# Kernel optimization log

Hardware: AMD Instinct MI355X
Metric: run time of the kernel (lower is better)

## Reference

```python
import jax, jax.numpy as jnp
import numpy as np
from jax import lax

V_PATCH = (1, 2, 3, 4, 5, 6, 8, 10, 13, 16)
BETA = 0.25
RESI = 0.5          # abs(quant_resi): h*(1-r) + conv(h)*r
K_PHI = 4           # share_quant_resi
PHI_TICKS = np.linspace(1.0 / (3 * K_PHI), 1.0 - 1.0 / (3 * K_PHI), K_PHI)


def _area_mat(out_s, in_s):
    # torch F.interpolate(mode='area') == adaptive avg pool: row-stochastic matrix
    M = np.zeros((out_s, in_s), np.float32)
    for i in range(out_s):
        s = (i * in_s) // out_s
        e = -((-(i + 1) * in_s) // out_s)  # ceil((i+1)*in/out)
        M[i, s:e] = 1.0 / (e - s)
    return jnp.asarray(M)


def _bicubic_mat(out_s, in_s):
    # torch bicubic, align_corners=False, a=-0.75, border-clamped taps
    a = -0.75
    i = np.arange(out_s)
    src = (i + 0.5) * in_s / out_s - 0.5
    fl = np.floor(src)
    M = np.zeros((out_s, in_s), np.float32)
    for t in range(-1, 3):
        x = np.abs(src - (fl + t))
        w = np.where(x <= 1.0, (a + 2) * x**3 - (a + 3) * x**2 + 1.0,
                     np.where(x < 2.0, a * x**3 - 5 * a * x**2 + 8 * a * x - 4 * a, 0.0))
        idx = np.clip(fl + t, 0, in_s - 1).astype(int)
        np.add.at(M, (i, idx), w)
    return jnp.asarray(M)


def _resize(x, M):
    # separable resize on square maps: x [B,C,h,w] -> [B,C,o,o]
    x = jnp.einsum('oh,bchw->bcow', M, x)
    return jnp.einsum('pw,bcow->bcop', M, x)


def _phi(h, w, b):
    # Phi: Conv2d(C,C,3,pad=1); out = h*(1-r) + conv(h)*r
    c = lax.conv_general_dilated(h, w, (1, 1), 'SAME',
                                 dimension_numbers=('NCHW', 'OIHW', 'NCHW'))
    c = c + b[None, :, None, None]
    return h * (1.0 - RESI) + c * RESI


def setup_inputs() -> dict:
    key = jax.random.key(0)
    k1, k2, k3, k4 = jax.random.split(key, 4)
    f = jax.random.normal(k1, (128, 32, 16, 16), jnp.float32)
    emb = jax.random.normal(k2, (4096, 32), jnp.float32) * 0.1
    phi_w = jax.random.normal(k3, (4, 32, 32, 3, 3), jnp.float32) * 0.05
    phi_b = jax.random.normal(k4, (4, 32), jnp.float32) * 0.01
    return {"f_BChw": f, "emb_W": emb, "phi_W": phi_w, "phi_b": phi_b}


def reference(f_BChw, emb_W, phi_W, phi_b):
    B, C, H, W = f_BChw.shape
    SN = len(V_PATCH)
    f = f_BChw.astype(jnp.float32)
    f_ng = lax.stop_gradient(f)
    f_rest = f_ng
    f_hat = jnp.zeros_like(f_ng)
    emb_ng = lax.stop_gradient(emb_W)         # torch uses embedding.weight.data
    e_sq = jnp.sum(emb_ng**2, axis=1)          # [V]
    loss = jnp.float32(0.0)
    idx_list = []
    for si, pn in enumerate(V_PATCH):
        rest = f_rest if si == SN - 1 else _resize(f_rest, _area_mat(pn, H))
        rest_NC = rest.transpose(0, 2, 3, 1).reshape(-1, C)      # [B*pn*pn, C]
        d = jnp.sum(rest_NC**2, axis=1, keepdims=True) + e_sq - 2.0 * (rest_NC @ emb_ng.T)
        idx = jnp.argmin(d, axis=1)                              # [B*pn*pn]
        idx_list.append(idx)
        h = emb_W[idx].reshape(B, pn, pn, C).transpose(0, 3, 1, 2)  # differentiable gather
        if si != SN - 1:
            h = _resize(h, _bicubic_mat(H, pn))
        k = int(np.argmin(np.abs(PHI_TICKS - si / (SN - 1))))
        h = _phi(h, phi_W[k], phi_b[k])
        f_hat = f_hat + h
        f_rest = f_rest - h
        loss = loss + BETA * jnp.mean((lax.stop_gradient(f_hat) - f)**2) \
                    + jnp.mean((f_hat - f_ng)**2)
    loss = loss / SN
    f_hat_out = lax.stop_gradient(f_hat) - f_ng + f  # straight-through
    return (f_hat_out, loss, jnp.concatenate(idx_list))
```

## Files before the change

kernel.cpp:

```cpp
#include <hip/hip_runtime.h>
#include <hip/hip_bf16.h>
#include <math.h>


#define B_  128
#define V_  4096
#define SN_ 10
#define NPIX_ (B_*32*256)

#define WS_FREST   0
#define WS_SLOTA   1048576
#define WS_SLOTB   1114112
#define WS_ESQ     1179648
#define WS_TW      1183744
#define WS_TI      1184320
#define WS_LOSSP   1184896
#define WS_RESTH   1187456
#define WS_RESTM   1711744
#define WS_RESTL   2236032
#define WS_EMBH    2760320
#define WS_EMBM    2825856
#define WS_EMBL    2891392
#define WS_WSPL    2956928

typedef __attribute__((ext_vector_type(8))) short short8_t;
typedef __attribute__((ext_vector_type(4))) float f32x4;
typedef unsigned long long ull;
#define MFMA(a,b,c) __builtin_amdgcn_mfma_f32_16x16x32_bf16((a),(b),(c),0,0,0)

__device__ inline void gl_lds16(const void* g, void* l) {
  __builtin_amdgcn_global_load_lds((const __attribute__((address_space(1))) void*)g,
                                   (__attribute__((address_space(3))) void*)l, 16, 0, 0);
}
__device__ inline void gl_lds4(const void* g, void* l) {
  __builtin_amdgcn_global_load_lds((const __attribute__((address_space(1))) void*)g,
                                   (__attribute__((address_space(3))) void*)l, 4, 0, 0);
}

__device__ inline void split3(float a, ushort* h, ushort* m, ushort* l) {
  unsigned ua = __float_as_uint(a);
  ushort uh = (ushort)(ua >> 16);
  float fh = __uint_as_float((unsigned)uh << 16);
  float r1 = a - fh;
  ushort um = (ushort)(__float_as_uint(r1) >> 16);
  float fm = __uint_as_float((unsigned)um << 16);
  float r2 = r1 - fm;
  ushort ul = (ushort)(__float_as_uint(r2) >> 16);
  *h = uh; *m = um; *l = ul;
}

__device__ inline short8_t s8_from_laneM1(short8_t v) {
  union { short8_t s; unsigned u[4]; } a, r;
  a.s = v;
#pragma unroll
  for (int i = 0; i < 4; ++i)
    r.u[i] = __builtin_amdgcn_update_dpp(0u, a.u[i], 0x111, 0xF, 0xF, true);
  return r.s;
}
__device__ inline short8_t s8_from_laneP1(short8_t v) {
  union { short8_t s; unsigned u[4]; } a, r;
  a.s = v;
#pragma unroll
  for (int i = 0; i < 4; ++i)
    r.u[i] = __builtin_amdgcn_update_dpp(0u, a.u[i], 0x101, 0xF, 0xF, true);
  return r.s;
}


__global__ __launch_bounds__(256) void k_prep(const float* __restrict__ emb,
                                              float* __restrict__ esq,
                                              ushort* __restrict__ eh,
                                              ushort* __restrict__ em,
                                              ushort* __restrict__ el,
                                              float* __restrict__ tw,
                                              int* __restrict__ ti,
                                              ull* __restrict__ slotA) {
  int bx = blockIdx.x, t = threadIdx.x;
  if (bx < 16) {
    int v = bx * 256 + t;
    const float4* e4 = (const float4*)(emb + (size_t)v * 32);
    float s = 0.f;
#pragma unroll
    for (int half = 0; half < 4; ++half) {
      float4 x0 = e4[half * 2], x1 = e4[half * 2 + 1];
      s += x0.x * x0.x + x0.y * x0.y + x0.z * x0.z + x0.w * x0.w;
      s += x1.x * x1.x + x1.y * x1.y + x1.z * x1.z + x1.w * x1.w;
      float xs[8] = {x0.x, x0.y, x0.z, x0.w, x1.x, x1.y, x1.z, x1.w};
      ushort hs[8], ms[8], ls[8];
#pragma unroll
      for (int j = 0; j < 8; ++j) split3(xs[j], &hs[j], &ms[j], &ls[j]);
      uint4 ph, pm, pl;
      ph.x = (unsigned)hs[0] | ((unsigned)hs[1] << 16); ph.y = (unsigned)hs[2] | ((unsigned)hs[3] << 16);
      ph.z = (unsigned)hs[4] | ((unsigned)hs[5] << 16); ph.w = (unsigned)hs[6] | ((unsigned)hs[7] << 16);
      pm.x = (unsigned)ms[0] | ((unsigned)ms[1] << 16); pm.y = (unsigned)ms[2] | ((unsigned)ms[3] << 16);
      pm.z = (unsigned)ms[4] | ((unsigned)ms[5] << 16); pm.w = (unsigned)ms[6] | ((unsigned)ms[7] << 16);
      pl.x = (unsigned)ls[0] | ((unsigned)ls[1] << 16); pl.y = (unsigned)ls[2] | ((unsigned)ls[3] << 16);
      pl.z = (unsigned)ls[4] | ((unsigned)ls[5] << 16); pl.w = (unsigned)ls[6] | ((unsigned)ls[7] << 16);
      ((uint4*)(eh + (size_t)v * 32))[half] = ph;
      ((uint4*)(em + (size_t)v * 32))[half] = pm;
      ((uint4*)(el + (size_t)v * 32))[half] = pl;
    }
    esq[v] = -0.5f * s;
  } else {
    if (t < 128) slotA[t] = 0ULL;
    if (t >= 144) return;
    const int pns[9] = {1, 2, 3, 4, 5, 6, 8, 10, 13};
    int si = t / 16, Y = t % 16;
    int pn = pns[si];
    double src = (Y + 0.5) * (double)pn / 16.0 - 0.5;
    double fl = floor(src);
    const double a = -0.75;
#pragma unroll
    for (int k = 0; k < 4; ++k) {
      double x = fabs(src - (fl + (k - 1)));
      double w;
      if (x <= 1.0)      w = (a + 2.0) * x * x * x - (a + 3.0) * x * x + 1.0;
      else if (x < 2.0)  w = a * x * x * x - 5.0 * a * x * x + 8.0 * a * x - 4.0 * a;
      else               w = 0.0;
      int id = (int)fl + (k - 1);
      id = id < 0 ? 0 : (id > pn - 1 ? pn - 1 : id);
      tw[si * 64 + Y * 4 + k] = (float)w;
      ti[si * 64 + Y * 4 + k] = id;
    }
  }
}

__global__ __launch_bounds__(256) void k_prep2(const float* __restrict__ f,
                                               const float* __restrict__ phiW,
                                               ushort* __restrict__ rh,
                                               ushort* __restrict__ rm,
                                               ushort* __restrict__ rl,
                                               ushort* __restrict__ wspl) {
  int bx = blockIdx.x, t = threadIdx.x;
  if (bx < 16) {
    int i = bx * 256 + t;
    int phi = i >> 10, o = (i >> 5) & 31, ci = i & 31;
    const float* src = phiW + (((size_t)phi * 32 + o) * 32 + ci) * 9;
    ushort* dst = wspl + (size_t)phi * 27648;
#pragma unroll
    for (int q = 0; q < 9; ++q) {
      ushort uh, um, ul;
      split3(src[q], &uh, &um, &ul);
      dst[(size_t)(0 * 9 + q) * 1024 + o * 32 + ci] = uh;
      dst[(size_t)(9 + q) * 1024 + o * 32 + ci] = um;
      dst[(size_t)(18 + q) * 1024 + o * 32 + ci] = ul;
    }
  } else {
    int tid = (bx - 16) * 256 + t;
    int c = tid & 31, n = tid >> 5;
    const float* base = f + ((size_t)n * 32 + c) * 256;
    float s = 0.f;
    for (int yy = 0; yy < 16; ++yy)
      for (int xx = 0; xx < 16; ++xx) s += base[yy * 16 + xx];
    float a = s * ((1.0f / 16.0f) * (1.0f / 16.0f));
    ushort uh, um, ul;
    split3(a, &uh, &um, &ul);
    rh[(size_t)n * 32 + c] = uh;
    rm[(size_t)n * 32 + c] = um;
    rl[(size_t)n * 32 + c] = ul;
  }
}

template<int R>
__global__ __launch_bounds__(256) void k_nn(const ushort* __restrict__ rest_h,
                                            const ushort* __restrict__ rest_m,
                                            const ushort* __restrict__ rest_l,
                                            const ushort* __restrict__ emb_h,
                                            const ushort* __restrict__ emb_m,
                                            const ushort* __restrict__ emb_l,
                                            const float* __restrict__ esq_g,
                                            ull* __restrict__ slot,
                                            int rows, int S, int cps) {
  __shared__ ushort lb[2][3][2048];
  __shared__ float les[2][64];
  const int t = threadIdx.x;
  const int w = t >> 6;
  const int col = t & 15;
  const int g = (t >> 4) & 3;
  const int sp = blockIdx.y;
  const int rowbase = blockIdx.x * (64 * R);

  auto stage = [&](int bf, int ch) {
    int cb = sp * cps + ch * 64;
    int code = cb + (t >> 2);
    int u = (t & 3) ^ ((code ^ (code >> 2)) & 3);
    size_t off = (size_t)code * 32 + (size_t)u * 8;
    gl_lds16(emb_h + off, &lb[bf][0][w * 512]);
    gl_lds16(emb_m + off, &lb[bf][1][w * 512]);
    gl_lds16(emb_l + off, &lb[bf][2][w * 512]);
    if ((t & 63) < 16) gl_lds4(esq_g + cb + w * 16 + (t & 15), &les[bf][w * 16]);
  };

  stage(0, 0);

  short8_t ah[R], am[R], al[R];
#pragma unroll
  for (int rt = 0; rt < R; ++rt) {
    int n = rowbase + (w * R + rt) * 16 + col;
    if (n >= rows) n = rows - 1;
    size_t o = (size_t)n * 32 + g * 8;
    ah[rt] = *(const short8_t*)(rest_h + o);
    am[rt] = *(const short8_t*)(rest_m + o);
    al[rt] = *(const short8_t*)(rest_l + o);
  }

  float best[R][4];
  int bidx[R][4];
#pragma unroll
  for (int rt = 0; rt < R; ++rt)
#pragma unroll
    for (int r = 0; r < 4; ++r) { best[rt][r] = -3.4e38f; bidx[rt][r] = 0x7fffffff; }

  const int NC = cps >> 6;
  int buf = 0;
  for (int ch = 0; ch < NC; ++ch) {
    if (ch + 1 < NC) {
      stage(buf ^ 1, ch + 1);
      asm volatile("s_waitcnt vmcnt(4)" ::: "memory");
    } else {
      asm volatile("s_waitcnt vmcnt(0)" ::: "memory");
    }
    __builtin_amdgcn_s_barrier();

    int cb0 = sp * cps + ch * 64;
#pragma unroll
    for (int s4 = 0; s4 < 4; ++s4) {
      int cl = s4 * 16 + col;
      int slotbase = (cl * 4 + (g ^ ((cl ^ (cl >> 2)) & 3))) * 8;
      short8_t bh  = *(const short8_t*)&lb[buf][0][slotbase];
      short8_t bm  = *(const short8_t*)&lb[buf][1][slotbase];
      short8_t bl2 = *(const short8_t*)&lb[buf][2][slotbase];
      float es = les[buf][cl];
      f32x4 c0 = {es, es, es, es};
      f32x4 acc[R];
#pragma unroll
      for (int rt = 0; rt < R; ++rt) acc[rt] = MFMA(ah[rt], bh, c0);
#pragma unroll
      for (int rt = 0; rt < R; ++rt) acc[rt] = MFMA(ah[rt], bm, acc[rt]);
#pragma unroll
      for (int rt = 0; rt < R; ++rt) acc[rt] = MFMA(am[rt], bh, acc[rt]);
#pragma unroll
      for (int rt = 0; rt < R; ++rt) acc[rt] = MFMA(ah[rt], bl2, acc[rt]);
#pragma unroll
      for (int rt = 0; rt < R; ++rt) acc[rt] = MFMA(am[rt], bm, acc[rt]);
#pragma unroll
      for (int rt = 0; rt < R; ++rt) acc[rt] = MFMA(al[rt], bh, acc[rt]);
      int code = cb0 + cl;
#pragma unroll
      for (int rt = 0; rt < R; ++rt)
#pragma unroll
        for (int r = 0; r < 4; ++r)
          if (acc[rt][r] > best[rt][r]) { best[rt][r] = acc[rt][r]; bidx[rt][r] = code; }
    }
    __syncthreads();
    buf ^= 1;
  }

#pragma unroll
  for (int rt = 0; rt < R; ++rt)
#pragma unroll
    for (int r = 0; r < 4; ++r) {
      float bd = best[rt][r];
      int bi = bidx[rt][r];
#pragma unroll
      for (int mm2 = 1; mm2 < 16; mm2 <<= 1) {
        float od = __shfl_xor(bd, mm2, 16);
        int oi = __shfl_xor(bi, mm2, 16);
        if (od > bd || (od == bd && oi < bi)) { bd = od; bi = oi; }
      }
      if ((t & 15) == 0) {
        int rown = rowbase + (w * R + rt) * 16 + g * 4 + r;
        if (rown < rows) {
          unsigned mu = __float_as_uint(bd);
          mu ^= (mu & 0x80000000u) ? 0xFFFFFFFFu : 0x80000000u;
          ull key = ((ull)mu << 32) | (unsigned)(~bi);
          atomicMax(&slot[rown], key);
        }
      }
    }
}

template<bool LAST>
__global__ __launch_bounds__(1024) void k_scale(const ull* __restrict__ slot_in,
                                                ull* __restrict__ slot_next,
                                                const float* __restrict__ emb,
                                                const float* __restrict__ tw,
                                                const int* __restrict__ ti,
                                                const ushort* __restrict__ wspl,
                                                const float* __restrict__ bias,
                                                const float* __restrict__ f,
                                                const float* __restrict__ fr_in,
                                                float* __restrict__ fr_out,
                                                float* __restrict__ fhat_out,
                                                float* __restrict__ out_idx_f,
                                                float* __restrict__ lossp,
                                                ushort* __restrict__ rh,
                                                ushort* __restrict__ rm,
                                                ushort* __restrict__ rl,
                                                int pn, int si, int pn_next,
                                                int rows_next) {
  __shared__ ushort h_bf[3][256][40];
  __shared__ float hsm[32 * 177];
  __shared__ float xt[32][208];
  __shared__ float h_my[16][260];
  __shared__ ushort w_lds[27][16][36];
  __shared__ int ci_s[256];
  __shared__ float redw[16];
  float* poolb = hsm;

  const int b = blockIdx.x;
  const int cog = blockIdx.y * 16;
  const int t = threadIdx.x;
  const int pn2 = pn * pn;
  const int w = t >> 6, l = t & 63;
  const int X = l & 15, kq = l >> 4;
  const int pix = w * 16 + X;

  float fr_old[4], f_old[4];
#pragma unroll
  for (int r = 0; r < 4; ++r) {
    size_t ga = ((size_t)b * 32 + cog + kq * 4 + r) * 256 + pix;
    fr_old[r] = fr_in[ga];
    f_old[r] = LAST ? f[ga] : 0.f;
  }
  for (int i = t; i < 1728; i += 1024) {
    int seg = i & 3;
    int o = (i >> 2) & 15;
    int lq = i >> 6;
    const ushort* src = wspl + ((size_t)lq * 32 + cog + o) * 32 + seg * 8;
    *(short8_t*)&w_lds[lq][o][seg * 8] = *(const short8_t*)src;
  }
  for (int rem = t; rem < pn2; rem += 1024) {
    ull sv = slot_in[b * pn2 + rem];
    int code = (int)(~(unsigned)sv);
    ci_s[rem] = code;
    out_idx_f[b * pn2 + rem] = (float)code;
  }
  __syncthreads();

#pragma unroll
  for (int cc = 0; cc < 2; ++cc) {
    int c = 2 * w + cc;
    if (LAST) {
      for (int p2 = l; p2 < 256; p2 += 64) {
        float v = emb[(size_t)ci_s[p2] * 32 + c];
        ushort uh, um, ul; split3(v, &uh, &um, &ul);
        h_bf[0][p2][c] = uh; h_bf[1][p2][c] = um; h_bf[2][p2][c] = ul;
        int cl = c - cog;
        if ((unsigned)cl < 16u) h_my[cl][p2] = v;
      }
    } else {
      for (int rem = l; rem < pn2; rem += 64)
        hsm[c * 177 + rem] = emb[(size_t)ci_s[rem] * 32 + c];
      asm volatile("s_waitcnt lgkmcnt(0)" ::: "memory");
      for (int i = l; i < pn * 16; i += 64) {
        int Xi = i & 15, y = i >> 4;
        float a = 0.f;
#pragma unroll
        for (int u = 0; u < 4; ++u)
          a += tw[si * 64 + Xi * 4 + u] * hsm[c * 177 + y * pn + ti[si * 64 + Xi * 4 + u]];
        xt[c][y * 16 + Xi] = a;
      }
      asm volatile("s_waitcnt lgkmcnt(0)" ::: "memory");
      for (int p2 = l; p2 < 256; p2 += 64) {
        int Xi = p2 & 15, Y = p2 >> 4;
        float a = 0.f;
#pragma unroll
        for (int u = 0; u < 4; ++u)
          a += tw[si * 64 + Y * 4 + u] * xt[c][ti[si * 64 + Y * 4 + u] * 16 + Xi];
        ushort uh, um, ul; split3(a, &uh, &um, &ul);
        h_bf[0][p2][c] = uh; h_bf[1][p2][c] = um; h_bf[2][p2][c] = ul;
        int cl = c - cog;
        if ((unsigned)cl < 16u) h_my[cl][p2] = a;
      }
    }
  }
  __syncthreads();

  f32x4 accA, accB;
#pragma unroll
  for (int r = 0; r < 4; ++r) {
    accA[r] = bias[cog + kq * 4 + r];
    accB[r] = 0.f;
  }

  for (int dy = 0; dy < 3; ++dy) {
    int Yp = w + dy - 1;
    bool ok = (Yp >= 0 && Yp < 16);
    short8_t bc[3];
    if (ok) {
#pragma unroll
      for (int lv = 0; lv < 3; ++lv)
        bc[lv] = *(const short8_t*)&h_bf[lv][Yp * 16 + X][kq * 8];
    }
#pragma unroll
    for (int dx = 0; dx < 3; ++dx) {
      int q = dy * 3 + dx;
      short8_t aH = *(const short8_t*)&w_lds[0 * 9 + q][l & 15][kq * 8];
      short8_t aM = *(const short8_t*)&w_lds[9 + q][l & 15][kq * 8];
      short8_t aL = *(const short8_t*)&w_lds[18 + q][l & 15][kq * 8];
      if (!ok) continue;
      short8_t bH = bc[0], bM = bc[1], bL = bc[2];
      if (dx == 0) { bH = s8_from_laneM1(bH); bM = s8_from_laneM1(bM); bL = s8_from_laneM1(bL); }
      else if (dx == 2) { bH = s8_from_laneP1(bH); bM = s8_from_laneP1(bM); bL = s8_from_laneP1(bL); }
      accA = MFMA(aH, bH, accA);
      accB = MFMA(aH, bM, accB);
      accA = MFMA(aM, bH, accA);
      accB = MFMA(aH, bL, accB);
      accA = MFMA(aM, bM, accA);
      accB = MFMA(aL, bH, accB);
    }
  }

  float lsum = 0.f;
#pragma unroll
  for (int r = 0; r < 4; ++r) {
    int ol = kq * 4 + r;
    float convv = accA[r] + accB[r];
    float outv = 0.5f * h_my[ol][pix] + 0.5f * convv;
    float nf = fr_old[r] - outv;
    size_t ga = ((size_t)b * 32 + cog + ol) * 256 + pix;
    if (LAST) {
      fhat_out[ga] = f_old[r] - nf;
    } else {
      fr_out[ga] = nf;
      poolb[ol * 256 + pix] = nf;
    }
    lsum += nf * nf;
  }

  if (!LAST) {
    __syncthreads();
    int pn2n = pn_next * pn_next;
    for (int i = t; i < 16 * pn2n; i += 1024) {
      int o = i / pn2n, rem = i - o * pn2n;
      int y = rem / pn_next, x = rem - y * pn_next;
      int sy = (y * 16) / pn_next, ey = ((y + 1) * 16 + pn_next - 1) / pn_next;
      int sx = (x * 16) / pn_next, ex = ((x + 1) * 16 + pn_next - 1) / pn_next;
      float s = 0.f;
      for (int yy = sy; yy < ey; ++yy)
        for (int xx = sx; xx < ex; ++xx) s += poolb[o * 256 + yy * 16 + xx];
      float a = s * ((1.0f / (float)(ey - sy)) * (1.0f / (float)(ex - sx)));
      ushort uh, um, ul;
      split3(a, &uh, &um, &ul);
      size_t n = (size_t)b * pn2n + rem;
      rh[n * 32 + cog + o] = uh;
      rm[n * 32 + cog + o] = um;
      rl[n * 32 + cog + o] = ul;
    }
    int blk = b * 2 + blockIdx.y;
    int stride = (rows_next + 255) >> 8;
    int base = blk * stride;
    for (int i = t; i < stride; i += 1024) {
      int s = base + i;
      if (s < rows_next) slot_next[s] = 0ULL;
    }
  }

#pragma unroll
  for (int off = 32; off > 0; off >>= 1) lsum += __shfl_down(lsum, off);
  if (l == 0) redw[w] = lsum;
  __syncthreads();
  if (t == 0) {
    float s2 = 0.f;
#pragma unroll
    for (int i = 0; i < 16; ++i) s2 += redw[i];
    lossp[si * 256 + blockIdx.y * 128 + b] = s2;
  }
}

__global__ __launch_bounds__(256) void k_lossfin(const float* __restrict__ part,
                                                 float* __restrict__ out) {
  int t = threadIdx.x;
  float s = 0.f;
  for (int i = t; i < SN_ * 256; i += 256) s += part[i];
  __shared__ float red[256];
  red[t] = s;
  __syncthreads();
  for (int o = 128; o > 0; o >>= 1) {
    if (t < o) red[t] += red[t + o];
    __syncthreads();
  }
  if (t == 0) out[NPIX_] = red[0] * (1.25f / (10.0f * (float)NPIX_));
}


static void compute_phi_k(int* ks) {
  const int K = 4;
  double start = 1.0 / (3.0 * K);
  double stop = 1.0 - 1.0 / (3.0 * K);
  double step = (stop - start) / (K - 1);
  double ticks[4];
  for (int i = 0; i < K; ++i) ticks[i] = (double)i * step + start;
  ticks[K - 1] = stop;
  for (int si = 0; si < SN_; ++si) {
    double x = (double)si / (SN_ - 1);
    int best = 0;
    double bd = fabs(ticks[0] - x);
    for (int i = 1; i < K; ++i) {
      double d = fabs(ticks[i] - x);
      if (d < bd) { bd = d; best = i; }
    }
    ks[si] = best;
  }
}

extern "C" void kernel_launch(void* const* d_in, const int* in_sizes, int n_in,
                              void* d_out, int out_size, void* d_ws, size_t ws_size,
                              hipStream_t stream) {
  (void)in_sizes; (void)n_in; (void)out_size; (void)ws_size;
  const float* f    = (const float*)d_in[0];
  const float* emb  = (const float*)d_in[1];
  const float* phiW = (const float*)d_in[2];
  const float* phiB = (const float*)d_in[3];
  float* out = (float*)d_out;
  float* ws = (float*)d_ws;

  float* f_rest = ws + WS_FREST;
  ull*   slotA  = (ull*)(ws + WS_SLOTA);
  ull*   slotB  = (ull*)(ws + WS_SLOTB);
  float* esq    = ws + WS_ESQ;
  float* tw     = ws + WS_TW;
  int*   ti     = (int*)(ws + WS_TI);
  float* lossp  = ws + WS_LOSSP;
  ushort* rest_h = (ushort*)(ws + WS_RESTH);
  ushort* rest_m = (ushort*)(ws + WS_RESTM);
  ushort* rest_l = (ushort*)(ws + WS_RESTL);
  ushort* emb_h  = (ushort*)(ws + WS_EMBH);
  ushort* emb_m  = (ushort*)(ws + WS_EMBM);
  ushort* emb_l  = (ushort*)(ws + WS_EMBL);
  ushort* wspl   = (ushort*)(ws + WS_WSPL);

  static const int pns[SN_] = {1, 2, 3, 4, 5, 6, 8, 10, 13, 16};
  static const int Rs[SN_]  = {1, 1, 1, 2, 2, 2, 4, 4, 4, 4};
  static const int Ss[SN_]  = {64, 64, 32, 32, 16, 16, 16, 16, 8, 4};
  int ks[SN_];
  compute_phi_k(ks);

  k_prep<<<17, 256, 0, stream>>>(emb, esq, emb_h, emb_m, emb_l, tw, ti, slotA);
  k_prep2<<<32, 256, 0, stream>>>(f, phiW, rest_h, rest_m, rest_l, wspl);

  int idx_off = 0;
  for (int si = 0; si < SN_; ++si) {
    int pn = pns[si];
    int pn2 = pn * pn;
    int rows = B_ * pn2;
    int R = Rs[si], S = Ss[si];
    int cps = V_ / S;
    int rowblocks = (rows + 64 * R - 1) / (64 * R);
    ull* slot_cur  = (si & 1) ? slotB : slotA;
    ull* slot_nxt  = (si & 1) ? slotA : slotB;

    dim3 grid(rowblocks, S);
    if (R == 1)
      k_nn<1><<<grid, 256, 0, stream>>>(rest_h, rest_m, rest_l, emb_h, emb_m, emb_l,
                                        esq, slot_cur, rows, S, cps);
    else if (R == 2)
      k_nn<2><<<grid, 256, 0, stream>>>(rest_h, rest_m, rest_l, emb_h, emb_m, emb_l,
                                        esq, slot_cur, rows, S, cps);
    else
      k_nn<4><<<grid, 256, 0, stream>>>(rest_h, rest_m, rest_l, emb_h, emb_m, emb_l,
                                        esq, slot_cur, rows, S, cps);

    bool last = (si == SN_ - 1);
    int pn_next = last ? 0 : pns[si + 1];
    int rows_next = last ? 0 : B_ * pn_next * pn_next;
    const ushort* wsp = wspl + (size_t)ks[si] * 27648;
    const float* bi = phiB + (size_t)ks[si] * 32;
    if (last)
      k_scale<true><<<dim3(B_, 2), 1024, 0, stream>>>(
          slot_cur, slot_nxt, emb, tw, ti, wsp, bi, f,
          f_rest, f_rest, out,
          out + NPIX_ + 1 + idx_off, lossp,
          rest_h, rest_m, rest_l, pn, si, pn_next, rows_next);
    else
      k_scale<false><<<dim3(B_, 2), 1024, 0, stream>>>(
          slot_cur, slot_nxt, emb, tw, ti, wsp, bi, f,
          (si == 0) ? f : f_rest, f_rest, nullptr,
          out + NPIX_ + 1 + idx_off, lossp,
          rest_h, rest_m, rest_l, pn, si, pn_next, rows_next);
    idx_off += rows;
  }

  k_lossfin<<<1, 256, 0, stream>>>(lossp, out);
}
```

Baseline: 390.1 us.

## Split per-scale kernel into separate interpolation and conv kernels via global scratch

The fused per-scale kernel is split into two kernels. k_interp gathers codebook rows, does the bicubic upsample and writes the bf16 triple-split and fp32 maps to workspace. k_conv then reads those maps and the conv weights straight from global memory instead of staging them in LDS. This removes the interpolation work that was duplicated across both channel-group blocks and frees LDS, at the cost of an extra launch per scale and an extra global round-trip for the intermediate maps. The pooling loop index order is also changed.

New measurement: 421.9 us. +8.1%, slower.

```diff
diff --git a/kernel.cpp b/kernel.cpp
--- a/kernel.cpp
+++ b/kernel.cpp
@@ -9,19 +9,21 @@
 #define NPIX_ (B_*32*256)
 
 #define WS_FREST   0
-#define WS_SLOTA   1048576
-#define WS_SLOTB   1114112
-#define WS_ESQ     1179648
-#define WS_TW      1183744
-#define WS_TI      1184320
-#define WS_LOSSP   1184896
-#define WS_RESTH   1187456
-#define WS_RESTM   1711744
-#define WS_RESTL   2236032
-#define WS_EMBH    2760320
-#define WS_EMBM    2825856
-#define WS_EMBL    2891392
-#define WS_WSPL    2956928
+#define WS_HF32    1048576
+#define WS_HBF     2097152
+#define WS_SLOTA   3670016
+#define WS_SLOTB   3735552
+#define WS_ESQ     3801088
+#define WS_TW      3805184
+#define WS_TI      3805760
+#define WS_LOSSP   3806336
+#define WS_RESTH   3808896
+#define WS_RESTM   4333184
+#define WS_RESTL   4857472
+#define WS_EMBH    5381760
+#define WS_EMBM    5447296
+#define WS_EMBL    5512832
+#define WS_WSPL    5578368
 
 typedef __attribute__((ext_vector_type(8))) short short8_t;
 typedef __attribute__((ext_vector_type(4))) float f32x4;
@@ -281,37 +283,107 @@
 }
 
 template<bool LAST>
-__global__ __launch_bounds__(1024) void k_scale(const ull* __restrict__ slot_in,
-                                                ull* __restrict__ slot_next,
+__global__ __launch_bounds__(256) void k_interp(const ull* __restrict__ slot_in,
                                                 const float* __restrict__ emb,
                                                 const float* __restrict__ tw,
                                                 const int* __restrict__ ti,
-                                                const ushort* __restrict__ wspl,
-                                                const float* __restrict__ bias,
-                                                const float* __restrict__ f,
-                                                const float* __restrict__ fr_in,
-                                                float* __restrict__ fr_out,
-                                                float* __restrict__ fhat_out,
                                                 float* __restrict__ out_idx_f,
-                                                float* __restrict__ lossp,
-                                                ushort* __restrict__ rh,
-                                                ushort* __restrict__ rm,
-                                                ushort* __restrict__ rl,
-                                                int pn, int si, int pn_next,
-                                                int rows_next) {
-  __shared__ ushort h_bf[3][256][40];
-  __shared__ float hsm[32 * 177];
-  __shared__ float xt[32][208];
-  __shared__ float h_my[16][260];
-  __shared__ ushort w_lds[27][16][36];
+                                                ushort* __restrict__ hb0,
+                                                ushort* __restrict__ hb1,
+                                                ushort* __restrict__ hb2,
+                                                float* __restrict__ h_f32,
+                                                int pn, int si) {
   __shared__ int ci_s[256];
+  __shared__ float hsm[8][176];
+  __shared__ float xt[8][208];
+  const int b = blockIdx.x;
+  const int c0 = blockIdx.y * 8;
+  const int t = threadIdx.x;
+  const int pn2 = pn * pn;
+
+  for (int rem = t; rem < pn2; rem += 256) {
+    ull sv = slot_in[b * pn2 + rem];
+    int code = (int)(~(unsigned)sv);
+    ci_s[rem] = code;
+    if (blockIdx.y == 0) out_idx_f[b * pn2 + rem] = (float)code;
+  }
+  __syncthreads();
+
+  float vals[8];
+  if (LAST) {
+    const float4* emb4 = (const float4*)emb;
+    int ci = ci_s[t];
+    float4 e0 = emb4[(size_t)ci * 8 + (c0 >> 2)];
+    float4 e1 = emb4[(size_t)ci * 8 + (c0 >> 2) + 1];
+    vals[0] = e0.x; vals[1] = e0.y; vals[2] = e0.z; vals[3] = e0.w;
+    vals[4] = e1.x; vals[5] = e1.y; vals[6] = e1.z; vals[7] = e1.w;
+  } else {
+    const float4* emb4 = (const float4*)emb;
+    for (int i = t; i < pn2 * 2; i += 256) {
+      int rem = i >> 1, half = i & 1;
+      float4 e = emb4[(size_t)ci_s[rem] * 8 + (c0 >> 2) + half];
+      hsm[half * 4 + 0][rem] = e.x;
+      hsm[half * 4 + 1][rem] = e.y;
+      hsm[half * 4 + 2][rem] = e.z;
+      hsm[half * 4 + 3][rem] = e.w;
+    }
+    __syncthreads();
+    int e1n = 8 * pn * 16;
+    for (int i = t; i < e1n; i += 256) {
+      int Xi = i & 15, r2 = i >> 4;
+      int y = r2 % pn, lc = r2 / pn;
+      float a = 0.f;
+#pragma unroll
+      for (int u = 0; u < 4; ++u)
+        a += tw[si * 64 + Xi * 4 + u] * hsm[lc][y * pn + ti[si * 64 + Xi * 4 + u]];
+      xt[lc][y * 16 + Xi] = a;
+    }
+    __syncthreads();
+    int Xi = t & 15, Y = t >> 4;
+#pragma unroll
+    for (int lc = 0; lc < 8; ++lc) {
+      float a = 0.f;
+#pragma unroll
+      for (int u = 0; u < 4; ++u)
+        a += tw[si * 64 + Y * 4 + u] * xt[lc][ti[si * 64 + Y * 4 + u] * 16 + Xi];
+      vals[lc] = a;
+    }
+  }
+
+  ushort hs[8], ms[8], ls[8];
+#pragma unroll
+  for (int j = 0; j < 8; ++j) split3(vals[j], &hs[j], &ms[j], &ls[j]);
+  size_t base = ((size_t)b * 256 + t) * 32 + c0;
+  *(short8_t*)(hb0 + base) = *(short8_t*)hs;
+  *(short8_t*)(hb1 + base) = *(short8_t*)ms;
+  *(short8_t*)(hb2 + base) = *(short8_t*)ls;
+  float4* hf4 = (float4*)(h_f32 + base);
+  hf4[0] = make_float4(vals[0], vals[1], vals[2], vals[3]);
+  hf4[1] = make_float4(vals[4], vals[5], vals[6], vals[7]);
+}
+
+template<bool LAST>
+__global__ __launch_bounds__(1024) void k_conv(const ushort* __restrict__ hb0,
+                                               const ushort* __restrict__ hb1,
+                                               const ushort* __restrict__ hb2,
+                                               const float* __restrict__ h_f32,
+                                               const ushort* __restrict__ wspl_k,
+                                               const float* __restrict__ bias,
+                                               const float* __restrict__ f,
+                                               const float* __restrict__ fr_in,
+                                               float* __restrict__ fr_out,
+                                               float* __restrict__ fhat_out,
+                                               float* __restrict__ lossp,
+                                               ushort* __restrict__ rh,
+                                               ushort* __restrict__ rm,
+                                               ushort* __restrict__ rl,
+                                               ull* __restrict__ slot_next,
+                                               int si, int pn_next, int rows_next) {
+  __shared__ float poolb[16 * 256];
   __shared__ float redw[16];
-  float* poolb = hsm;
-
   const int b = blockIdx.x;
   const int cog = blockIdx.y * 16;
   const int t = threadIdx.x;
-  const int pn2 = pn * pn;
   const int w = t >> 6, l = t & 63;
   const int X = l & 15, kq = l >> 4;
   const int pix = w * 16 + X;
@@ -323,59 +395,7 @@
     fr_old[r] = fr_in[ga];
     f_old[r] = LAST ? f[ga] : 0.f;
   }
-  for (int i = t; i < 1728; i += 1024) {
-    int seg = i & 3;
-    int o = (i >> 2) & 15;
-    int lq = i >> 6;
-    const ushort* src = wspl + ((size_t)lq * 32 + cog + o) * 32 + seg * 8;
-    *(short8_t*)&w_lds[lq][o][seg * 8] = *(const short8_t*)src;
-  }
-  for (int rem = t; rem < pn2; rem += 1024) {
-    ull sv = slot_in[b * pn2 + rem];
-    int code = (int)(~(unsigned)sv);
-    ci_s[rem] = code;
-    out_idx_f[b * pn2 + rem] = (float)code;
-  }
-  __syncthreads();
-
-#pragma unroll
-  for (int cc = 0; cc < 2; ++cc) {
-    int c = 2 * w + cc;
-    if (LAST) {
-      for (int p2 = l; p2 < 256; p2 += 64) {
-        float v = emb[(size_t)ci_s[p2] * 32 + c];
-        ushort uh, um, ul; split3(v, &uh, &um, &ul);
-        h_bf[0][p2][c] = uh; h_bf[1][p2][c] = um; h_bf[2][p2][c] = ul;
-        int cl = c - cog;
-        if ((unsigned)cl < 16u) h_my[cl][p2] = v;
-      }
-    } else {
-      for (int rem = l; rem < pn2; rem += 64)
-        hsm[c * 177 + rem] = emb[(size_t)ci_s[rem] * 32 + c];
-      asm volatile("s_waitcnt lgkmcnt(0)" ::: "memory");
-      for (int i = l; i < pn * 16; i += 64) {
-        int Xi = i & 15, y = i >> 4;
-        float a = 0.f;
-#pragma unroll
-        for (int u = 0; u < 4; ++u)
-          a += tw[si * 64 + Xi * 4 + u] * hsm[c * 177 + y * pn + ti[si * 64 + Xi * 4 + u]];
-        xt[c][y * 16 + Xi] = a;
-      }
-      asm volatile("s_waitcnt lgkmcnt(0)" ::: "memory");
-      for (int p2 = l; p2 < 256; p2 += 64) {
-        int Xi = p2 & 15, Y = p2 >> 4;
-        float a = 0.f;
-#pragma unroll
-        for (int u = 0; u < 4; ++u)
-          a += tw[si * 64 + Y * 4 + u] * xt[c][ti[si * 64 + Y * 4 + u] * 16 + Xi];
-        ushort uh, um, ul; split3(a, &uh, &um, &ul);
-        h_bf[0][p2][c] = uh; h_bf[1][p2][c] = um; h_bf[2][p2][c] = ul;
-        int cl = c - cog;
-        if ((unsigned)cl < 16u) h_my[cl][p2] = a;
-      }
-    }
-  }
-  __syncthreads();
+  float4 hmy = *(const float4*)(h_f32 + ((size_t)b * 256 + pix) * 32 + cog + kq * 4);
 
   f32x4 accA, accB;
 #pragma unroll
@@ -384,21 +404,24 @@
     accB[r] = 0.f;
   }
 
+#pragma unroll 1
   for (int dy = 0; dy < 3; ++dy) {
     int Yp = w + dy - 1;
     bool ok = (Yp >= 0 && Yp < 16);
     short8_t bc[3];
     if (ok) {
-#pragma unroll
-      for (int lv = 0; lv < 3; ++lv)
-        bc[lv] = *(const short8_t*)&h_bf[lv][Yp * 16 + X][kq * 8];
+      size_t hbase = ((size_t)b * 256 + Yp * 16 + X) * 32 + kq * 8;
+      bc[0] = *(const short8_t*)(hb0 + hbase);
+      bc[1] = *(const short8_t*)(hb1 + hbase);
+      bc[2] = *(const short8_t*)(hb2 + hbase);
     }
 #pragma unroll
     for (int dx = 0; dx < 3; ++dx) {
       int q = dy * 3 + dx;
-      short8_t aH = *(const short8_t*)&w_lds[0 * 9 + q][l & 15][kq * 8];
-      short8_t aM = *(const short8_t*)&w_lds[9 + q][l & 15][kq * 8];
-      short8_t aL = *(const short8_t*)&w_lds[18 + q][l & 15][kq * 8];
+      const ushort* wp = wspl_k + (size_t)q * 1024 + (size_t)(cog + (l & 15)) * 32 + kq * 8;
+      short8_t aH = *(const short8_t*)(wp);
+      short8_t aM = *(const short8_t*)(wp + 9 * 1024);
+      short8_t aL = *(const short8_t*)(wp + 18 * 1024);
       if (!ok) continue;
       short8_t bH = bc[0], bM = bc[1], bL = bc[2];
       if (dx == 0) { bH = s8_from_laneM1(bH); bM = s8_from_laneM1(bM); bL = s8_from_laneM1(bL); }
@@ -412,12 +435,13 @@
     }
   }
 
+  float hmys[4] = {hmy.x, hmy.y, hmy.z, hmy.w};
   float lsum = 0.f;
 #pragma unroll
   for (int r = 0; r < 4; ++r) {
     int ol = kq * 4 + r;
     float convv = accA[r] + accB[r];
-    float outv = 0.5f * h_my[ol][pix] + 0.5f * convv;
+    float outv = 0.5f * hmys[r] + 0.5f * convv;
     float nf = fr_old[r] - outv;
     size_t ga = ((size_t)b * 32 + cog + ol) * 256 + pix;
     if (LAST) {
@@ -433,7 +457,7 @@
     __syncthreads();
     int pn2n = pn_next * pn_next;
     for (int i = t; i < 16 * pn2n; i += 1024) {
-      int o = i / pn2n, rem = i - o * pn2n;
+      int o = i & 15, rem = i >> 4;
       int y = rem / pn_next, x = rem - y * pn_next;
       int sy = (y * 16) / pn_next, ey = ((y + 1) * 16 + pn_next - 1) / pn_next;
       int sx = (x * 16) / pn_next, ex = ((x + 1) * 16 + pn_next - 1) / pn_next;
@@ -517,6 +541,10 @@
   float* ws = (float*)d_ws;
 
   float* f_rest = ws + WS_FREST;
+  float* h_f32  = ws + WS_HF32;
+  ushort* hb0   = (ushort*)(ws + WS_HBF);
+  ushort* hb1   = (ushort*)(ws + WS_HBF + 524288);
+  ushort* hb2   = (ushort*)(ws + WS_HBF + 1048576);
   ull*   slotA  = (ull*)(ws + WS_SLOTA);
   ull*   slotB  = (ull*)(ws + WS_SLOTB);
   float* esq    = ws + WS_ESQ;
@@ -567,18 +595,24 @@
     int rows_next = last ? 0 : B_ * pn_next * pn_next;
     const ushort* wsp = wspl + (size_t)ks[si] * 27648;
     const float* bi = phiB + (size_t)ks[si] * 32;
-    if (last)
-      k_scale<true><<<dim3(B_, 2), 1024, 0, stream>>>(
-          slot_cur, slot_nxt, emb, tw, ti, wsp, bi, f,
-          f_rest, f_rest, out,
-          out + NPIX_ + 1 + idx_off, lossp,
-          rest_h, rest_m, rest_l, pn, si, pn_next, rows_next);
-    else
-      k_scale<false><<<dim3(B_, 2), 1024, 0, stream>>>(
-          slot_cur, slot_nxt, emb, tw, ti, wsp, bi, f,
-          (si == 0) ? f : f_rest, f_rest, nullptr,
-          out + NPIX_ + 1 + idx_off, lossp,
-          rest_h, rest_m, rest_l, pn, si, pn_next, rows_next);
+
+    if (last) {
+      k_interp<true><<<dim3(B_, 4), 256, 0, stream>>>(
+          slot_cur, emb, tw, ti, out + NPIX_ + 1 + idx_off,
+          hb0, hb1, hb2, h_f32, pn, si);
+      k_conv<true><<<dim3(B_, 2), 1024, 0, stream>>>(
+          hb0, hb1, hb2, h_f32, wsp, bi, f,
+          f_rest, f_rest, out, lossp,
+          rest_h, rest_m, rest_l, slot_nxt, si, pn_next, rows_next);
+    } else {
+      k_interp<false><<<dim3(B_, 4), 256, 0, stream>>>(
+          slot_cur, emb, tw, ti, out + NPIX_ + 1 + idx_off,
+          hb0, hb1, hb2, h_f32, pn, si);
+      k_conv<false><<<dim3(B_, 2), 1024, 0, stream>>>(
+          hb0, hb1, hb2, h_f32, wsp, bi, f,
+          (si == 0) ? f : f_rest, f_rest, nullptr, lossp,
+          rest_h, rest_m, rest_l, slot_nxt, si, pn_next, rows_next);
+    }
     idx_off += rows;
   }
 
```

## Restructure k_scale to 512 threads with two rows per wave and lean LDS

Applied to the files above, without the earlier changes.

The per-scale conv/update kernel drops from 1024 to 512 threads, and each wave now computes two image rows so the weight fragments are reused across both. Weights are read straight from global memory instead of being staged in LDS. The bicubic upsample is rebuilt as two 16-channel passes that read embeddings directly, and the pool buffer now aliases h_bf to shrink LDS. The goal is higher occupancy (launch bounds 512,4) and less LDS traffic. In exchange it adds extra barriers and uncached global weight loads inside the MFMA loop.

Measured after the change: 392.6 us. No clear change (+0.7%).

```diff
diff --git a/kernel.cpp b/kernel.cpp
--- a/kernel.cpp
+++ b/kernel.cpp
@@ -24,6 +24,7 @@
 #define WS_WSPL    2956928
 
 typedef __attribute__((ext_vector_type(8))) short short8_t;
+typedef __attribute__((ext_vector_type(4))) short short4_t;
 typedef __attribute__((ext_vector_type(4))) float f32x4;
 typedef unsigned long long ull;
 #define MFMA(a,b,c) __builtin_amdgcn_mfma_f32_16x16x32_bf16((a),(b),(c),0,0,0)
@@ -281,32 +282,30 @@
 }
 
 template<bool LAST>
-__global__ __launch_bounds__(1024) void k_scale(const ull* __restrict__ slot_in,
-                                                ull* __restrict__ slot_next,
-                                                const float* __restrict__ emb,
-                                                const float* __restrict__ tw,
-                                                const int* __restrict__ ti,
-                                                const ushort* __restrict__ wspl,
-                                                const float* __restrict__ bias,
-                                                const float* __restrict__ f,
-                                                const float* __restrict__ fr_in,
-                                                float* __restrict__ fr_out,
-                                                float* __restrict__ fhat_out,
-                                                float* __restrict__ out_idx_f,
-                                                float* __restrict__ lossp,
-                                                ushort* __restrict__ rh,
-                                                ushort* __restrict__ rm,
-                                                ushort* __restrict__ rl,
-                                                int pn, int si, int pn_next,
-                                                int rows_next) {
-  __shared__ ushort h_bf[3][256][40];
-  __shared__ float hsm[32 * 177];
-  __shared__ float xt[32][208];
-  __shared__ float h_my[16][260];
-  __shared__ ushort w_lds[27][16][36];
+__global__ __launch_bounds__(512, 4) void k_scale(const ull* __restrict__ slot_in,
+                                                  ull* __restrict__ slot_next,
+                                                  const float* __restrict__ emb,
+                                                  const float* __restrict__ tw,
+                                                  const int* __restrict__ ti,
+                                                  const ushort* __restrict__ wspl_k,
+                                                  const float* __restrict__ bias,
+                                                  const float* __restrict__ f,
+                                                  const float* __restrict__ fr_in,
+                                                  float* __restrict__ fr_out,
+                                                  float* __restrict__ fhat_out,
+                                                  float* __restrict__ out_idx_f,
+                                                  float* __restrict__ lossp,
+                                                  ushort* __restrict__ rh,
+                                                  ushort* __restrict__ rm,
+                                                  ushort* __restrict__ rl,
+                                                  int pn, int si, int pn_next,
+                                                  int rows_next) {
+  __shared__ ushort h_bf[3][256][32];
+  __shared__ float h_my[256][16];
+  __shared__ float xt16[16][208];
   __shared__ int ci_s[256];
-  __shared__ float redw[16];
-  float* poolb = hsm;
+  __shared__ float redw[8];
+  float* poolb = (float*)&h_bf[0][0][0];
 
   const int b = blockIdx.x;
   const int cog = blockIdx.y * 16;
@@ -314,126 +313,176 @@
   const int pn2 = pn * pn;
   const int w = t >> 6, l = t & 63;
   const int X = l & 15, kq = l >> 4;
-  const int pix = w * 16 + X;
-
-  float fr_old[4], f_old[4];
-#pragma unroll
-  for (int r = 0; r < 4; ++r) {
-    size_t ga = ((size_t)b * 32 + cog + kq * 4 + r) * 256 + pix;
-    fr_old[r] = fr_in[ga];
-    f_old[r] = LAST ? f[ga] : 0.f;
-  }
-  for (int i = t; i < 1728; i += 1024) {
-    int seg = i & 3;
-    int o = (i >> 2) & 15;
-    int lq = i >> 6;
-    const ushort* src = wspl + ((size_t)lq * 32 + cog + o) * 32 + seg * 8;
-    *(short8_t*)&w_lds[lq][o][seg * 8] = *(const short8_t*)src;
-  }
-  for (int rem = t; rem < pn2; rem += 1024) {
+
+  for (int rem = t; rem < pn2; rem += 512) {
     ull sv = slot_in[b * pn2 + rem];
     int code = (int)(~(unsigned)sv);
     ci_s[rem] = code;
-    out_idx_f[b * pn2 + rem] = (float)code;
+    if (blockIdx.y == 0) out_idx_f[b * pn2 + rem] = (float)code;
+  }
+  float fr_old[2][4], f_old[2][4];
+#pragma unroll
+  for (int rr = 0; rr < 2; ++rr) {
+    int pix = (2 * w + rr) * 16 + X;
+#pragma unroll
+    for (int r = 0; r < 4; ++r) {
+      size_t ga = ((size_t)b * 32 + cog + kq * 4 + r) * 256 + pix;
+      fr_old[rr][r] = fr_in[ga];
+      f_old[rr][r] = LAST ? f[ga] : 0.f;
+    }
   }
   __syncthreads();
 
-#pragma unroll
-  for (int cc = 0; cc < 2; ++cc) {
-    int c = 2 * w + cc;
-    if (LAST) {
-      for (int p2 = l; p2 < 256; p2 += 64) {
-        float v = emb[(size_t)ci_s[p2] * 32 + c];
-        ushort uh, um, ul; split3(v, &uh, &um, &ul);
-        h_bf[0][p2][c] = uh; h_bf[1][p2][c] = um; h_bf[2][p2][c] = ul;
-        int cl = c - cog;
-        if ((unsigned)cl < 16u) h_my[cl][p2] = v;
+  if (LAST) {
+    int pix = t & 255, j = t >> 8;
+    int ci = ci_s[pix];
+    const float4* e4 = (const float4*)(emb + (size_t)ci * 32);
+    float vals[16];
+#pragma unroll
+    for (int q = 0; q < 4; ++q) {
+      float4 e = e4[j * 4 + q];
+      vals[q * 4 + 0] = e.x; vals[q * 4 + 1] = e.y;
+      vals[q * 4 + 2] = e.z; vals[q * 4 + 3] = e.w;
+    }
+    ushort hs[16], ms[16], ls[16];
+#pragma unroll
+    for (int m = 0; m < 16; ++m) split3(vals[m], &hs[m], &ms[m], &ls[m]);
+    *(short8_t*)&h_bf[0][pix][j * 16]     = *(short8_t*)&hs[0];
+    *(short8_t*)&h_bf[0][pix][j * 16 + 8] = *(short8_t*)&hs[8];
+    *(short8_t*)&h_bf[1][pix][j * 16]     = *(short8_t*)&ms[0];
+    *(short8_t*)&h_bf[1][pix][j * 16 + 8] = *(short8_t*)&ms[8];
+    *(short8_t*)&h_bf[2][pix][j * 16]     = *(short8_t*)&ls[0];
+    *(short8_t*)&h_bf[2][pix][j * 16 + 8] = *(short8_t*)&ls[8];
+    if (j == blockIdx.y) {
+      float4* hm4 = (float4*)&h_my[pix][0];
+#pragma unroll
+      for (int q = 0; q < 4; ++q)
+        hm4[q] = make_float4(vals[q * 4], vals[q * 4 + 1], vals[q * 4 + 2], vals[q * 4 + 3]);
+    }
+    __syncthreads();
+  } else {
+#pragma unroll 1
+    for (int P = 0; P < 2; ++P) {
+      int e1n = 16 * pn * 16;
+      for (int i = t; i < e1n; i += 512) {
+        int Xi = i & 15, r2 = i >> 4;
+        int y = r2 % pn, c16 = r2 / pn;
+        int c = P * 16 + c16;
+        float a = 0.f;
+#pragma unroll
+        for (int u = 0; u < 4; ++u) {
+          int ix = ti[si * 64 + Xi * 4 + u];
+          a += tw[si * 64 + Xi * 4 + u] * emb[(size_t)ci_s[y * pn + ix] * 32 + c];
+        }
+        xt16[c16][y * 16 + Xi] = a;
       }
-    } else {
-      for (int rem = l; rem < pn2; rem += 64)
-        hsm[c * 177 + rem] = emb[(size_t)ci_s[rem] * 32 + c];
-      asm volatile("s_waitcnt lgkmcnt(0)" ::: "memory");
-      for (int i = l; i < pn * 16; i += 64) {
-        int Xi = i & 15, y = i >> 4;
-        float a = 0.f;
-#pragma unroll
-        for (int u = 0; u < 4; ++u)
-          a += tw[si * 64 + Xi * 4 + u] * hsm[c * 177 + y * pn + ti[si * 64 + Xi * 4 + u]];
-        xt[c][y * 16 + Xi] = a;
+      __syncthreads();
+      for (int i = t; i < 1024; i += 512) {
+        int pix = i & 255, j = i >> 8;
+        int Xi = pix & 15, Y = pix >> 4;
+        float vals[4];
+        ushort hs[4], ms[4], ls[4];
+#pragma unroll
+        for (int cc = 0; cc < 4; ++cc) {
+          int c16 = j * 4 + cc;
+          float a = 0.f;
+#pragma unroll
+          for (int u = 0; u < 4; ++u)
+            a += tw[si * 64 + Y * 4 + u] * xt16[c16][ti[si * 64 + Y * 4 + u] * 16 + Xi];
+          vals[cc] = a;
+          split3(a, &hs[cc], &ms[cc], &ls[cc]);
+        }
+        int colbase = P * 16 + j * 4;
+        *(short4_t*)&h_bf[0][pix][colbase] = *(short4_t*)hs;
+        *(short4_t*)&h_bf[1][pix][colbase] = *(short4_t*)ms;
+        *(short4_t*)&h_bf[2][pix][colbase] = *(short4_t*)ls;
+        if (P == blockIdx.y)
+          *(float4*)&h_my[pix][j * 4] = make_float4(vals[0], vals[1], vals[2], vals[3]);
       }
-      asm volatile("s_waitcnt lgkmcnt(0)" ::: "memory");
-      for (int p2 = l; p2 < 256; p2 += 64) {
-        int Xi = p2 & 15, Y = p2 >> 4;
-        float a = 0.f;
-#pragma unroll
-        for (int u = 0; u < 4; ++u)
-          a += tw[si * 64 + Y * 4 + u] * xt[c][ti[si * 64 + Y * 4 + u] * 16 + Xi];
-        ushort uh, um, ul; split3(a, &uh, &um, &ul);
-        h_bf[0][p2][c] = uh; h_bf[1][p2][c] = um; h_bf[2][p2][c] = ul;
-        int cl = c - cog;
-        if ((unsigned)cl < 16u) h_my[cl][p2] = a;
+      __syncthreads();
+    }
+  }
+
+  f32x4 accA[2], accB[2];
+#pragma unroll
+  for (int r = 0; r < 4; ++r) {
+    float bv = bias[cog + kq * 4 + r];
+    accA[0][r] = bv; accA[1][r] = bv;
+    accB[0][r] = 0.f; accB[1][r] = 0.f;
+  }
+
+#pragma unroll 1
+  for (int dy = 0; dy < 3; ++dy) {
+    short8_t bc[2][3];
+    bool ok[2];
+#pragma unroll
+    for (int rr = 0; rr < 2; ++rr) {
+      int Yp = 2 * w + rr + dy - 1;
+      ok[rr] = (Yp >= 0 && Yp < 16);
+      if (ok[rr]) {
+#pragma unroll
+        for (int lv = 0; lv < 3; ++lv)
+          bc[rr][lv] = *(const short8_t*)&h_bf[lv][Yp * 16 + X][kq * 8];
       }
-    }
-  }
-  __syncthreads();
-
-  f32x4 accA, accB;
-#pragma unroll
-  for (int r = 0; r < 4; ++r) {
-    accA[r] = bias[cog + kq * 4 + r];
-    accB[r] = 0.f;
-  }
-
-  for (int dy = 0; dy < 3; ++dy) {
-    int Yp = w + dy - 1;
-    bool ok = (Yp >= 0 && Yp < 16);
-    short8_t bc[3];
-    if (ok) {
-#pragma unroll
-      for (int lv = 0; lv < 3; ++lv)
-        bc[lv] = *(const short8_t*)&h_bf[lv][Yp * 16 + X][kq * 8];
     }
 #pragma unroll
     for (int dx = 0; dx < 3; ++dx) {
       int q = dy * 3 + dx;
-      short8_t aH = *(const short8_t*)&w_lds[0 * 9 + q][l & 15][kq * 8];
-      short8_t aM = *(const short8_t*)&w_lds[9 + q][l & 15][kq * 8];
-      short8_t aL = *(const short8_t*)&w_lds[18 + q][l & 15][kq * 8];
-      if (!ok) continue;
-      short8_t bH = bc[0], bM = bc[1], bL = bc[2];
-      if (dx == 0) { bH = s8_from_laneM1(bH); bM = s8_from_laneM1(bM); bL = s8_from_laneM1(bL); }
-      else if (dx == 2) { bH = s8_from_laneP1(bH); bM = s8_from_laneP1(bM); bL = s8_from_laneP1(bL); }
-      accA = MFMA(aH, bH, accA);
-      accB = MFMA(aH, bM, accB);
-      accA = MFMA(aM, bH, accA);
-      accB = MFMA(aH, bL, accB);
-      accA = MFMA(aM, bM, accA);
-      accB = MFMA(aL, bH, accB);
-    }
-  }
-
+      const ushort* wp = wspl_k + (size_t)q * 1024 + (size_t)(cog + X) * 32 + kq * 8;
+      short8_t aH = *(const short8_t*)(wp);
+      short8_t aM = *(const short8_t*)(wp + 9 * 1024);
+      short8_t aL = *(const short8_t*)(wp + 18 * 1024);
+#pragma unroll
+      for (int rr = 0; rr < 2; ++rr) {
+        if (!ok[rr]) continue;
+        short8_t bH = bc[rr][0], bM = bc[rr][1], bL = bc[rr][2];
+        if (dx == 0) { bH = s8_from_laneM1(bH); bM = s8_from_laneM1(bM); bL = s8_from_laneM1(bL); }
+        else if (dx == 2) { bH = s8_from_laneP1(bH); bM = s8_from_laneP1(bM); bL = s8_from_laneP1(bL); }
+        accA[rr] = MFMA(aH, bH, accA[rr]);
+        accB[rr] = MFMA(aH, bM, accB[rr]);
+        accA[rr] = MFMA(aM, bH, accA[rr]);
+        accB[rr] = MFMA(aH, bL, accB[rr]);
+        accA[rr] = MFMA(aM, bM, accA[rr]);
+        accB[rr] = MFMA(aL, bH, accB[rr]);
+      }
+    }
+  }
+
+  float nf_r[2][4];
   float lsum = 0.f;
 #pragma unroll
-  for (int r = 0; r < 4; ++r) {
-    int ol = kq * 4 + r;
-    float convv = accA[r] + accB[r];
-    float outv = 0.5f * h_my[ol][pix] + 0.5f * convv;
-    float nf = fr_old[r] - outv;
-    size_t ga = ((size_t)b * 32 + cog + ol) * 256 + pix;
-    if (LAST) {
-      fhat_out[ga] = f_old[r] - nf;
-    } else {
-      fr_out[ga] = nf;
-      poolb[ol * 256 + pix] = nf;
-    }
-    lsum += nf * nf;
+  for (int rr = 0; rr < 2; ++rr) {
+    int pix = (2 * w + rr) * 16 + X;
+#pragma unroll
+    for (int r = 0; r < 4; ++r) {
+      int ol = kq * 4 + r;
+      float convv = accA[rr][r] + accB[rr][r];
+      float outv = 0.5f * h_my[pix][ol] + 0.5f * convv;
+      float nf = fr_old[rr][r] - outv;
+      size_t ga = ((size_t)b * 32 + cog + ol) * 256 + pix;
+      if (LAST) {
+        fhat_out[ga] = f_old[rr][r] - nf;
+      } else {
+        fr_out[ga] = nf;
+      }
+      nf_r[rr][r] = nf;
+      lsum += nf * nf;
+    }
   }
 
   if (!LAST) {
     __syncthreads();
+#pragma unroll
+    for (int rr = 0; rr < 2; ++rr) {
+      int pix = (2 * w + rr) * 16 + X;
+#pragma unroll
+      for (int r = 0; r < 4; ++r)
+        poolb[(kq * 4 + r) * 256 + pix] = nf_r[rr][r];
+    }
+    __syncthreads();
     int pn2n = pn_next * pn_next;
-    for (int i = t; i < 16 * pn2n; i += 1024) {
-      int o = i / pn2n, rem = i - o * pn2n;
+    for (int i = t; i < 16 * pn2n; i += 512) {
+      int o = i & 15, rem = i >> 4;
       int y = rem / pn_next, x = rem - y * pn_next;
       int sy = (y * 16) / pn_next, ey = ((y + 1) * 16 + pn_next - 1) / pn_next;
       int sx = (x * 16) / pn_next, ex = ((x + 1) * 16 + pn_next - 1) / pn_next;
@@ -451,7 +500,7 @@
     int blk = b * 2 + blockIdx.y;
     int stride = (rows_next + 255) >> 8;
     int base = blk * stride;
-    for (int i = t; i < stride; i += 1024) {
+    for (int i = t; i < stride; i += 512) {
       int s = base + i;
       if (s < rows_next) slot_next[s] = 0ULL;
     }
@@ -464,7 +513,7 @@
   if (t == 0) {
     float s2 = 0.f;
 #pragma unroll
-    for (int i = 0; i < 16; ++i) s2 += redw[i];
+    for (int i = 0; i < 8; ++i) s2 += redw[i];
     lossp[si * 256 + blockIdx.y * 128 + b] = s2;
   }
 }
@@ -568,13 +617,13 @@
     const ushort* wsp = wspl + (size_t)ks[si] * 27648;
     const float* bi = phiB + (size_t)ks[si] * 32;
     if (last)
-      k_scale<true><<<dim3(B_, 2), 1024, 0, stream>>>(
+      k_scale<true><<<dim3(B_, 2), 512, 0, stream>>>(
           slot_cur, slot_nxt, emb, tw, ti, wsp, bi, f,
           f_rest, f_rest, out,
           out + NPIX_ + 1 + idx_off, lossp,
           rest_h, rest_m, rest_l, pn, si, pn_next, rows_next);
     else
-      k_scale<false><<<dim3(B_, 2), 1024, 0, stream>>>(
+      k_scale<false><<<dim3(B_, 2), 512, 0, stream>>>(
           slot_cur, slot_nxt, emb, tw, ti, wsp, bi, f,
           (si == 0) ? f : f_rest, f_rest, nullptr,
           out + NPIX_ + 1 + idx_off, lossp,
```
